# Optimization experiments

Measured on AMD Instinct MI355X. Metric: run time of the kernel, lower is better.

Reference implementation:

```python
import jax, jax.numpy as jnp
import numpy as np

EPS = 1e-3
FORGET_BIAS = 1.0


def layer_norm_groups(hmat, n_groups, num_units, gamma, beta):
    # hmat: [B, n_groups*num_units]; normalize each group of num_units independently
    B = hmat.shape[0]
    hr = hmat.reshape(B, n_groups, num_units)
    mean = hr.mean(axis=2, keepdims=True)
    var = ((hr - mean) ** 2).mean(axis=2, keepdims=True)
    hr = (hr - mean) * jax.lax.rsqrt(var + EPS)
    return gamma * hr.reshape(B, n_groups * num_units) + beta


def setup_inputs() -> dict:
    key = jax.random.key(0)
    ks = jax.random.split(key, 5)
    B, I, H = 8192, 1024, 1024
    return {
        "x": jax.random.normal(ks[0], (B, I), jnp.float32),
        "c": jax.random.normal(ks[1], (B, H), jnp.float32),
        "h": jax.random.normal(ks[2], (B, H), jnp.float32),
        "W_xh": jax.random.normal(ks[3], (I, 4 * H), jnp.float32) / np.sqrt(I),
        "W_hh": jax.random.normal(ks[4], (H, 4 * H), jnp.float32) / np.sqrt(H),
        "bias": jnp.zeros((4 * H,), jnp.float32),
        "ln_gamma": jnp.ones((4 * H,), jnp.float32),
        "ln_beta": jnp.zeros((4 * H,), jnp.float32),
        "ln_c_gamma": jnp.ones((H,), jnp.float32),
        "ln_c_beta": jnp.zeros((H,), jnp.float32),
    }


def reference(x, c, h, W_xh, W_hh, bias, ln_gamma, ln_beta, ln_c_gamma, ln_c_beta):
    H = c.shape[1]
    # fused gate matmul: cat([x,h]) @ cat([W_xh,W_hh]) == x@W_xh + h@W_hh
    concat = x @ W_xh + h @ W_hh + bias  # [B, 4H]
    concat = layer_norm_groups(concat, 4, H, ln_gamma, ln_beta)
    i, j, f, o = jnp.split(concat, 4, axis=1)
    new_c = c * jax.nn.sigmoid(f + FORGET_BIAS) + jax.nn.sigmoid(i) * jnp.tanh(j)
    c_ln = layer_norm_groups(new_c, 1, H, ln_c_gamma, ln_c_beta)
    new_h = jnp.tanh(c_ln) * jax.nn.sigmoid(o)
    return new_h, new_c
```

## Files before the change

### kernel.cpp

```cpp
#include <hip/hip_runtime.h>
#include <stdint.h>

#define Mdim 8192
#define Ndim 4096
#define Kdim 2048
#define Hdim 1024

typedef __attribute__((ext_vector_type(8))) short bf16x8;
typedef __attribute__((ext_vector_type(4))) float f32x4;

__device__ __forceinline__ unsigned short f2bf(float f) {
  union { float f; unsigned u; } v; v.f = f;
  unsigned u = v.u + 0x7fffu + ((v.u >> 16) & 1u);
  return (unsigned short)(u >> 16);
}
__device__ __forceinline__ float bf2f(unsigned short s) {
  union { unsigned u; float f; } v; v.u = ((unsigned)s) << 16;
  return v.f;
}
__device__ __forceinline__ float sigmoidf_(float x) { return 1.f / (1.f + __expf(-x)); }
__device__ __forceinline__ float tanhf_(float x) { return 1.f - 2.f / (1.f + __expf(2.f * x)); }

__global__ void conv_a_kernel(const float* __restrict__ x, const float* __restrict__ h,
                              unsigned short* __restrict__ A) {
  int idx = blockIdx.x * 256 + threadIdx.x;
  int m = idx >> 8;
  int k = (idx & 255) * 8;
  const float* src = (k < Hdim) ? (x + (size_t)m * Hdim + k)
                                : (h + (size_t)m * Hdim + (k - Hdim));
  float4 a = ((const float4*)src)[0];
  float4 b = ((const float4*)src)[1];
  union { unsigned short s[8]; int4 v; } o;
  o.s[0] = f2bf(a.x); o.s[1] = f2bf(a.y); o.s[2] = f2bf(a.z); o.s[3] = f2bf(a.w);
  o.s[4] = f2bf(b.x); o.s[5] = f2bf(b.y); o.s[6] = f2bf(b.z); o.s[7] = f2bf(b.w);
  *(int4*)(A + (size_t)idx * 8) = o.v;
}

__global__ void conv_w_kernel(const float* __restrict__ Wxh, const float* __restrict__ Whh,
                              unsigned short* __restrict__ Wt) {
  __shared__ float tile[32][33];
  int k0 = blockIdx.x * 32;
  int n0 = blockIdx.y * 32;
  int tx = threadIdx.x & 31, ty = threadIdx.x >> 5;
#pragma unroll
  for (int i = 0; i < 32; i += 8) {
    int k = k0 + ty + i;
    float v = (k < Hdim) ? Wxh[(size_t)k * Ndim + n0 + tx]
                         : Whh[(size_t)(k - Hdim) * Ndim + n0 + tx];
    tile[ty + i][tx] = v;
  }
  __syncthreads();
#pragma unroll
  for (int i = 0; i < 32; i += 8) {
    int n = n0 + ty + i;
    Wt[(size_t)n * Kdim + k0 + tx] = f2bf(tile[tx][ty + i]);
  }
}

#define BM 256
#define BN 256
#define BK 64
#define NT (Kdim / BK)

__global__ __launch_bounds__(512, 2)
void gemm_kernel(const unsigned short* __restrict__ A, const unsigned short* __restrict__ Bt,
                 unsigned short* __restrict__ C) {
  __shared__ unsigned short lds[2][2][BM * BK];
  const int tid = threadIdx.x;
  int bid = blockIdx.x;
  int id = (bid & 7) * 64 + (bid >> 3);
  int mT = id >> 4, nT = id & 15;
  size_t m0 = (size_t)mT * BM, n0 = (size_t)nT * BN;
  const int lane = tid & 63, w = tid >> 6;
  const int wm = w >> 2, wn = w & 3;
  const int r16 = lane & 15, q = lane >> 4;

  const unsigned short* gA = A + m0 * Kdim;
  const unsigned short* gB = Bt + n0 * Kdim;

  auto stage = [&](int b, int kt, int region) {
    const int mat = region >> 1, half = region & 1;
    const unsigned short* g = mat ? gB : gA;
#pragma unroll
    for (int it = 0; it < 2; ++it) {
      int c = it * 512 + tid;
      int rr = c >> 3, ss = c & 7;
      __builtin_amdgcn_global_load_lds(
          (const __attribute__((address_space(1))) void*)(
              g + (size_t)(half * 128 + rr) * Kdim + kt * BK + ((ss ^ (rr & 7)) << 3)),
          (__attribute__((address_space(3))) void*)(&lds[b][mat][half * (128 * BK) + c * 8]),
          16, 0, 0);
    }
  };

  f32x4 acc[8][4] = {};
  bf16x8 av0[4][2], av1[4][2], bv0[2][2], bv1[2][2];

  auto readA = [&](int cur, int mh, bf16x8 (&av)[4][2]) {
#pragma unroll
    for (int mi = 0; mi < 4; ++mi) {
      int lr = wm * 128 + mh * 64 + mi * 16 + r16;
      const unsigned short* base = &lds[cur][0][lr * BK];
#pragma unroll
      for (int ks = 0; ks < 2; ++ks)
        av[mi][ks] = *(const bf16x8*)(base + ((((ks << 2) | q) ^ (lr & 7)) << 3));
    }
  };
  auto readB = [&](int cur, int nh, bf16x8 (&bv)[2][2]) {
#pragma unroll
    for (int ni = 0; ni < 2; ++ni) {
      int lr = wn * 64 + nh * 32 + ni * 16 + r16;
      const unsigned short* base = &lds[cur][1][lr * BK];
#pragma unroll
      for (int ks = 0; ks < 2; ++ks)
        bv[ni][ks] = *(const bf16x8*)(base + ((((ks << 2) | q) ^ (lr & 7)) << 3));
    }
  };

#define QUAD(AV, BV, MI0, NI0)                                                        \
  do {                                                                                \
    __builtin_amdgcn_s_setprio(1);                                                    \
    _Pragma("unroll") for (int mi = 0; mi < 4; ++mi)                                  \
      _Pragma("unroll") for (int ni = 0; ni < 2; ++ni)                                \
        _Pragma("unroll") for (int ks = 0; ks < 2; ++ks)                              \
          acc[(MI0) + mi][(NI0) + ni] = __builtin_amdgcn_mfma_f32_16x16x32_bf16(      \
              AV[mi][ks], BV[ni][ks], acc[(MI0) + mi][(NI0) + ni], 0, 0, 0);          \
    __builtin_amdgcn_s_setprio(0);                                                    \
  } while (0)

  stage(0, 0, 0); stage(0, 0, 1); stage(0, 0, 2); stage(0, 0, 3);
  stage(1, 1, 0); stage(1, 1, 1);
  asm volatile("s_waitcnt vmcnt(4)" ::: "memory");
  __builtin_amdgcn_s_barrier();

#pragma unroll 2
  for (int t = 0; t < NT - 2; ++t) {
    int cur = t & 1, nxt = cur ^ 1;
    readA(cur, 0, av0);
    readB(cur, 0, bv0);
    stage(nxt, t + 1, 2);
    __builtin_amdgcn_s_barrier();
    QUAD(av0, bv0, 0, 0);
    __builtin_amdgcn_s_barrier();
    readA(cur, 1, av1);
    stage(nxt, t + 1, 3);
    __builtin_amdgcn_s_barrier();
    QUAD(av1, bv0, 4, 0);
    __builtin_amdgcn_s_barrier();
    readB(cur, 1, bv1);
    stage(cur, t + 2, 0);
    __builtin_amdgcn_s_barrier();
    QUAD(av1, bv1, 4, 2);
    __builtin_amdgcn_s_barrier();
    stage(cur, t + 2, 1);
    asm volatile("s_waitcnt vmcnt(4)" ::: "memory");
    __builtin_amdgcn_s_barrier();
    QUAD(av0, bv1, 0, 2);
    __builtin_amdgcn_s_barrier();
  }
  {
    const int cur = (NT - 2) & 1, nxt = cur ^ 1;
    readA(cur, 0, av0);
    readB(cur, 0, bv0);
    stage(nxt, NT - 1, 2);
    __builtin_amdgcn_s_barrier();
    QUAD(av0, bv0, 0, 0);
    __builtin_amdgcn_s_barrier();
    readA(cur, 1, av1);
    stage(nxt, NT - 1, 3);
    __builtin_amdgcn_s_barrier();
    QUAD(av1, bv0, 4, 0);
    __builtin_amdgcn_s_barrier();
    readB(cur, 1, bv1);
    __builtin_amdgcn_s_barrier();
    QUAD(av1, bv1, 4, 2);
    __builtin_amdgcn_s_barrier();
    asm volatile("s_waitcnt vmcnt(0)" ::: "memory");
    __builtin_amdgcn_s_barrier();
    QUAD(av0, bv1, 0, 2);
    __builtin_amdgcn_s_barrier();
  }
  {
    const int cur = (NT - 1) & 1;
    readA(cur, 0, av0);
    readB(cur, 0, bv0);
    QUAD(av0, bv0, 0, 0);
    readA(cur, 1, av1);
    QUAD(av1, bv0, 4, 0);
    readB(cur, 1, bv1);
    QUAD(av1, bv1, 4, 2);
    QUAD(av0, bv1, 0, 2);
  }
#undef QUAD

#pragma unroll
  for (int mi = 0; mi < 8; ++mi) {
#pragma unroll
    for (int ni = 0; ni < 4; ++ni) {
      size_t row = m0 + wm * 128 + mi * 16 + q * 4;
      size_t col = n0 + wn * 64 + ni * 16 + r16;
#pragma unroll
      for (int j = 0; j < 4; ++j)
        C[(row + j) * Ndim + col] = f2bf(acc[mi][ni][j]);
    }
  }
}

__global__ __launch_bounds__(256)
void tail_kernel(const unsigned short* __restrict__ Cc, const float* __restrict__ cin,
                 const float* __restrict__ bias, const float* __restrict__ gamma,
                 const float* __restrict__ beta, const float* __restrict__ cg,
                 const float* __restrict__ cb, float* __restrict__ out) {
  int lane = threadIdx.x & 63;
  int wid = threadIdx.x >> 6;
  int row = blockIdx.x * 4 + wid;
  const int base = lane * 16;

  const float4* cp = (const float4*)(cin + (size_t)row * Hdim + base);
  float4 c0 = cp[0], c1 = cp[1], c2 = cp[2], c3 = cp[3];
  float cv[16] = {c0.x, c0.y, c0.z, c0.w, c1.x, c1.y, c1.z, c1.w,
                  c2.x, c2.y, c2.z, c2.w, c3.x, c3.y, c3.z, c3.w};

  float accv[16];
  float ov[16];

#pragma unroll
  for (int g = 0; g < 4; ++g) {
    const int4* pp = (const int4*)(Cc + (size_t)row * Ndim + g * Hdim + base);
    int4 u0 = pp[0], u1 = pp[1];
    float vals[16];
    {
      int uu[8] = {u0.x, u0.y, u0.z, u0.w, u1.x, u1.y, u1.z, u1.w};
#pragma unroll
      for (int i = 0; i < 8; ++i) {
        vals[2 * i]     = bf2f((unsigned short)(uu[i] & 0xffff));
        vals[2 * i + 1] = bf2f((unsigned short)(((unsigned)uu[i]) >> 16));
      }
    }
    const float* bp = bias + g * Hdim + base;
#pragma unroll
    for (int t = 0; t < 16; ++t) vals[t] += bp[t];
    float s = 0.f, ss = 0.f;
#pragma unroll
    for (int t = 0; t < 16; ++t) { s += vals[t]; ss += vals[t] * vals[t]; }
#pragma unroll
    for (int off = 32; off; off >>= 1) { s += __shfl_xor(s, off); ss += __shfl_xor(ss, off); }
    float mean = s * (1.f / 1024.f);
    float rstd = rsqrtf(ss * (1.f / 1024.f) - mean * mean + 1e-3f);
    const float* gp = gamma + g * Hdim + base;
    const float* bb = beta + g * Hdim + base;
    if (g == 0) {
#pragma unroll
      for (int t = 0; t < 16; ++t)
        accv[t] = sigmoidf_((vals[t] - mean) * rstd * gp[t] + bb[t]);
    } else if (g == 1) {
#pragma unroll
      for (int t = 0; t < 16; ++t)
        accv[t] *= tanhf_((vals[t] - mean) * rstd * gp[t] + bb[t]);
    } else if (g == 2) {
#pragma unroll
      for (int t = 0; t < 16; ++t)
        accv[t] = cv[t] * sigmoidf_((vals[t] - mean) * rstd * gp[t] + bb[t] + 1.f) + accv[t];
    } else {
#pragma unroll
      for (int t = 0; t < 16; ++t)
        ov[t] = sigmoidf_((vals[t] - mean) * rstd * gp[t] + bb[t]);
    }
  }

  float s = 0.f, ss = 0.f;
#pragma unroll
  for (int t = 0; t < 16; ++t) { s += accv[t]; ss += accv[t] * accv[t]; }
#pragma unroll
  for (int off = 32; off; off >>= 1) { s += __shfl_xor(s, off); ss += __shfl_xor(ss, off); }
  float mean = s * (1.f / 1024.f);
  float rstd = rsqrtf(ss * (1.f / 1024.f) - mean * mean + 1e-3f);

  const float* cgp = cg + base;
  const float* cbp = cb + base;
  float hv[16];
#pragma unroll
  for (int t = 0; t < 16; ++t) {
    float cl = (accv[t] - mean) * rstd * cgp[t] + cbp[t];
    hv[t] = tanhf_(cl) * ov[t];
  }

  float4* oh = (float4*)(out + (size_t)row * Hdim + base);
  float4* oc = (float4*)(out + (size_t)Mdim * Hdim + (size_t)row * Hdim + base);
#pragma unroll
  for (int v = 0; v < 4; ++v) {
    oh[v] = make_float4(hv[4 * v], hv[4 * v + 1], hv[4 * v + 2], hv[4 * v + 3]);
    oc[v] = make_float4(accv[4 * v], accv[4 * v + 1], accv[4 * v + 2], accv[4 * v + 3]);
  }
}

extern "C" void kernel_launch(void* const* d_in, const int* in_sizes, int n_in,
                              void* d_out, int out_size, void* d_ws, size_t ws_size,
                              hipStream_t stream) {
  const float* x    = (const float*)d_in[0];
  const float* c    = (const float*)d_in[1];
  const float* h    = (const float*)d_in[2];
  const float* Wxh  = (const float*)d_in[3];
  const float* Whh  = (const float*)d_in[4];
  const float* bias = (const float*)d_in[5];
  const float* lng  = (const float*)d_in[6];
  const float* lnb  = (const float*)d_in[7];
  const float* cg   = (const float*)d_in[8];
  const float* cb   = (const float*)d_in[9];
  float* out = (float*)d_out;

  unsigned short* Abf = (unsigned short*)d_ws;
  unsigned short* Wt  = Abf + (size_t)Mdim * Kdim;
  unsigned short* Cc  = Wt  + (size_t)Ndim * Kdim;

  conv_a_kernel<<<8192, 256, 0, stream>>>(x, h, Abf);
  conv_w_kernel<<<dim3(Kdim / 32, Ndim / 32), 256, 0, stream>>>(Wxh, Whh, Wt);
  gemm_kernel<<<(Mdim / BM) * (Ndim / BN), 512, 0, stream>>>(Abf, Wt, Cc);
  tail_kernel<<<Mdim / 4, 256, 0, stream>>>(Cc, c, bias, lng, lnb, cg, cb, out);
}
```

Measured before the change: 214.4 us.

## Switch GEMM to 32x32x16 MFMA tiles and merge packing kernels

The GEMM inner loop moves from 16x16x32 bf16 MFMA to 32x32x16 bf16 MFMA. Each wave now holds 4x2 f32x16 accumulators, and the LDS fragment reads and the epilogue store mapping change to match. The larger MFMA is meant to raise math density per LDS read and cut instruction issue overhead. Separately, the activation and weight bf16 conversion kernels are merged into one launch to save a kernel launch. The 32-row output layout changes the store pattern, which may be less coalesced.

```diff
diff --git a/kernel.cpp b/kernel.cpp
--- a/kernel.cpp
+++ b/kernel.cpp
@@ -8,6 +8,7 @@
 
 typedef __attribute__((ext_vector_type(8))) short bf16x8;
 typedef __attribute__((ext_vector_type(4))) float f32x4;
+typedef __attribute__((ext_vector_type(16))) float f32x16;
 
 __device__ __forceinline__ unsigned short f2bf(float f) {
   union { float f; unsigned u; } v; v.f = f;
@@ -21,26 +22,27 @@
 __device__ __forceinline__ float sigmoidf_(float x) { return 1.f / (1.f + __expf(-x)); }
 __device__ __forceinline__ float tanhf_(float x) { return 1.f - 2.f / (1.f + __expf(2.f * x)); }
 
-__global__ void conv_a_kernel(const float* __restrict__ x, const float* __restrict__ h,
-                              unsigned short* __restrict__ A) {
-  int idx = blockIdx.x * 256 + threadIdx.x;
-  int m = idx >> 8;
-  int k = (idx & 255) * 8;
-  const float* src = (k < Hdim) ? (x + (size_t)m * Hdim + k)
-                                : (h + (size_t)m * Hdim + (k - Hdim));
-  float4 a = ((const float4*)src)[0];
-  float4 b = ((const float4*)src)[1];
-  union { unsigned short s[8]; int4 v; } o;
-  o.s[0] = f2bf(a.x); o.s[1] = f2bf(a.y); o.s[2] = f2bf(a.z); o.s[3] = f2bf(a.w);
-  o.s[4] = f2bf(b.x); o.s[5] = f2bf(b.y); o.s[6] = f2bf(b.z); o.s[7] = f2bf(b.w);
-  *(int4*)(A + (size_t)idx * 8) = o.v;
-}
-
-__global__ void conv_w_kernel(const float* __restrict__ Wxh, const float* __restrict__ Whh,
-                              unsigned short* __restrict__ Wt) {
+__global__ void pack_kernel(const float* __restrict__ x, const float* __restrict__ h,
+                            const float* __restrict__ Wxh, const float* __restrict__ Whh,
+                            unsigned short* __restrict__ A, unsigned short* __restrict__ Wt) {
+  if (blockIdx.x < 8192) {
+    int idx = blockIdx.x * 256 + threadIdx.x;
+    int m = idx >> 8;
+    int k = (idx & 255) * 8;
+    const float* src = (k < Hdim) ? (x + (size_t)m * Hdim + k)
+                                  : (h + (size_t)m * Hdim + (k - Hdim));
+    float4 a = ((const float4*)src)[0];
+    float4 b = ((const float4*)src)[1];
+    union { unsigned short s[8]; int4 v; } o;
+    o.s[0] = f2bf(a.x); o.s[1] = f2bf(a.y); o.s[2] = f2bf(a.z); o.s[3] = f2bf(a.w);
+    o.s[4] = f2bf(b.x); o.s[5] = f2bf(b.y); o.s[6] = f2bf(b.z); o.s[7] = f2bf(b.w);
+    *(int4*)(A + (size_t)idx * 8) = o.v;
+    return;
+  }
   __shared__ float tile[32][33];
-  int k0 = blockIdx.x * 32;
-  int n0 = blockIdx.y * 32;
+  int b2 = blockIdx.x - 8192;
+  int k0 = (b2 & 63) * 32;
+  int n0 = (b2 >> 6) * 32;
   int tx = threadIdx.x & 31, ty = threadIdx.x >> 5;
 #pragma unroll
   for (int i = 0; i < 32; i += 8) {
@@ -73,7 +75,7 @@
   size_t m0 = (size_t)mT * BM, n0 = (size_t)nT * BN;
   const int lane = tid & 63, w = tid >> 6;
   const int wm = w >> 2, wn = w & 3;
-  const int r16 = lane & 15, q = lane >> 4;
+  const int r32 = lane & 31, q2 = lane >> 5;
 
   const unsigned short* gA = A + m0 * Kdim;
   const unsigned short* gB = Bt + n0 * Kdim;
@@ -93,38 +95,34 @@
     }
   };
 
-  f32x4 acc[8][4] = {};
-  bf16x8 av0[4][2], av1[4][2], bv0[2][2], bv1[2][2];
-
-  auto readA = [&](int cur, int mh, bf16x8 (&av)[4][2]) {
-#pragma unroll
-    for (int mi = 0; mi < 4; ++mi) {
-      int lr = wm * 128 + mh * 64 + mi * 16 + r16;
+  f32x16 acc[4][2] = {};
+  bf16x8 av0[2][4], av1[2][4], bv0[4], bv1[4];
+
+  auto readA = [&](int cur, int mh, bf16x8 (&av)[2][4]) {
+#pragma unroll
+    for (int mf = 0; mf < 2; ++mf) {
+      int lr = wm * 128 + mh * 64 + mf * 32 + r32;
       const unsigned short* base = &lds[cur][0][lr * BK];
 #pragma unroll
-      for (int ks = 0; ks < 2; ++ks)
-        av[mi][ks] = *(const bf16x8*)(base + ((((ks << 2) | q) ^ (lr & 7)) << 3));
+      for (int ks = 0; ks < 4; ++ks)
+        av[mf][ks] = *(const bf16x8*)(base + ((((ks << 1) | q2) ^ (lr & 7)) << 3));
     }
   };
-  auto readB = [&](int cur, int nh, bf16x8 (&bv)[2][2]) {
-#pragma unroll
-    for (int ni = 0; ni < 2; ++ni) {
-      int lr = wn * 64 + nh * 32 + ni * 16 + r16;
-      const unsigned short* base = &lds[cur][1][lr * BK];
-#pragma unroll
-      for (int ks = 0; ks < 2; ++ks)
-        bv[ni][ks] = *(const bf16x8*)(base + ((((ks << 2) | q) ^ (lr & 7)) << 3));
-    }
+  auto readB = [&](int cur, int nh, bf16x8 (&bv)[4]) {
+    int lr = wn * 64 + nh * 32 + r32;
+    const unsigned short* base = &lds[cur][1][lr * BK];
+#pragma unroll
+    for (int ks = 0; ks < 4; ++ks)
+      bv[ks] = *(const bf16x8*)(base + ((((ks << 1) | q2) ^ (lr & 7)) << 3));
   };
 
 #define QUAD(AV, BV, MI0, NI0)                                                        \
   do {                                                                                \
     __builtin_amdgcn_s_setprio(1);                                                    \
-    _Pragma("unroll") for (int mi = 0; mi < 4; ++mi)                                  \
-      _Pragma("unroll") for (int ni = 0; ni < 2; ++ni)                                \
-        _Pragma("unroll") for (int ks = 0; ks < 2; ++ks)                              \
-          acc[(MI0) + mi][(NI0) + ni] = __builtin_amdgcn_mfma_f32_16x16x32_bf16(      \
-              AV[mi][ks], BV[ni][ks], acc[(MI0) + mi][(NI0) + ni], 0, 0, 0);          \
+    _Pragma("unroll") for (int mf = 0; mf < 2; ++mf)                                  \
+      _Pragma("unroll") for (int ks = 0; ks < 4; ++ks)                                \
+        acc[(MI0) + mf][NI0] = __builtin_amdgcn_mfma_f32_32x32x16_bf16(               \
+            AV[mf][ks], BV[ks], acc[(MI0) + mf][NI0], 0, 0, 0);                       \
     __builtin_amdgcn_s_setprio(0);                                                    \
   } while (0)
 
@@ -145,17 +143,17 @@
     readA(cur, 1, av1);
     stage(nxt, t + 1, 3);
     __builtin_amdgcn_s_barrier();
-    QUAD(av1, bv0, 4, 0);
+    QUAD(av1, bv0, 2, 0);
     __builtin_amdgcn_s_barrier();
     readB(cur, 1, bv1);
     stage(cur, t + 2, 0);
     __builtin_amdgcn_s_barrier();
-    QUAD(av1, bv1, 4, 2);
+    QUAD(av1, bv1, 2, 1);
     __builtin_amdgcn_s_barrier();
     stage(cur, t + 2, 1);
     asm volatile("s_waitcnt vmcnt(4)" ::: "memory");
     __builtin_amdgcn_s_barrier();
-    QUAD(av0, bv1, 0, 2);
+    QUAD(av0, bv1, 0, 1);
     __builtin_amdgcn_s_barrier();
   }
   {
@@ -169,15 +167,15 @@
     readA(cur, 1, av1);
     stage(nxt, NT - 1, 3);
     __builtin_amdgcn_s_barrier();
-    QUAD(av1, bv0, 4, 0);
+    QUAD(av1, bv0, 2, 0);
     __builtin_amdgcn_s_barrier();
     readB(cur, 1, bv1);
     __builtin_amdgcn_s_barrier();
-    QUAD(av1, bv1, 4, 2);
+    QUAD(av1, bv1, 2, 1);
     __builtin_amdgcn_s_barrier();
     asm volatile("s_waitcnt vmcnt(0)" ::: "memory");
     __builtin_amdgcn_s_barrier();
-    QUAD(av0, bv1, 0, 2);
+    QUAD(av0, bv1, 0, 1);
     __builtin_amdgcn_s_barrier();
   }
   {
@@ -186,22 +184,24 @@
     readB(cur, 0, bv0);
     QUAD(av0, bv0, 0, 0);
     readA(cur, 1, av1);
-    QUAD(av1, bv0, 4, 0);
+    QUAD(av1, bv0, 2, 0);
     readB(cur, 1, bv1);
-    QUAD(av1, bv1, 4, 2);
-    QUAD(av0, bv1, 0, 2);
+    QUAD(av1, bv1, 2, 1);
+    QUAD(av0, bv1, 0, 1);
   }
 #undef QUAD
 
 #pragma unroll
-  for (int mi = 0; mi < 8; ++mi) {
-#pragma unroll
-    for (int ni = 0; ni < 4; ++ni) {
-      size_t row = m0 + wm * 128 + mi * 16 + q * 4;
-      size_t col = n0 + wn * 64 + ni * 16 + r16;
-#pragma unroll
-      for (int j = 0; j < 4; ++j)
-        C[(row + j) * Ndim + col] = f2bf(acc[mi][ni][j]);
+  for (int mf = 0; mf < 4; ++mf) {
+#pragma unroll
+    for (int nf = 0; nf < 2; ++nf) {
+      size_t rb = m0 + wm * 128 + mf * 32 + q2 * 4;
+      size_t col = n0 + wn * 64 + nf * 32 + r32;
+#pragma unroll
+      for (int reg = 0; reg < 16; ++reg) {
+        size_t row = rb + (reg & 3) + 8 * (reg >> 2);
+        C[row * Ndim + col] = f2bf(acc[mf][nf][reg]);
+      }
     }
   }
 }
@@ -313,8 +313,7 @@
   unsigned short* Wt  = Abf + (size_t)Mdim * Kdim;
   unsigned short* Cc  = Wt  + (size_t)Ndim * Kdim;
 
-  conv_a_kernel<<<8192, 256, 0, stream>>>(x, h, Abf);
-  conv_w_kernel<<<dim3(Kdim / 32, Ndim / 32), 256, 0, stream>>>(Wxh, Whh, Wt);
+  pack_kernel<<<16384, 256, 0, stream>>>(x, h, Wxh, Whh, Abf, Wt);
   gemm_kernel<<<(Mdim / BM) * (Ndim / BN), 512, 0, stream>>>(Abf, Wt, Cc);
   tail_kernel<<<Mdim / 4, 256, 0, stream>>>(Cc, c, bias, lng, lnb, cg, cb, out);
 }
```

Result: slower. 229.0 us (+6.8%).
